# Optimization experiments

Measured on AMD Instinct MI355X. Metric: run time of the kernel, lower is better.

The kernel has to match this reference:

```python
import jax, jax.numpy as jnp
import numpy as np

IN_FEATURES = 4096
OUT_FEATURES = 11008
GROUP_SIZE = 128
NBITS = 4
ALPHA = 0.05  # relative noise scale: sigma = ALPHA * |w|


def setup_inputs() -> dict:
    key = jax.random.key(0)
    k_x, k_q, k_s, k_z, k_b, k_n = jax.random.split(key, 6)
    n_groups = IN_FEATURES // GROUP_SIZE  # 32
    x = jax.random.normal(k_x, (4096, IN_FEATURES), dtype=jnp.float32)
    qweight = jax.random.randint(k_q, (OUT_FEATURES, IN_FEATURES), 0, 2 ** NBITS, dtype=jnp.int32)
    scales = jax.random.uniform(k_s, (OUT_FEATURES, n_groups), dtype=jnp.float32) * 0.01 + 1e-4
    zeros = jax.random.uniform(k_z, (OUT_FEATURES, n_groups), dtype=jnp.float32) * (2 ** NBITS)
    bias = jax.random.normal(k_b, (OUT_FEATURES,), dtype=jnp.float32)
    noise = jax.random.normal(k_n, (OUT_FEATURES, IN_FEATURES), dtype=jnp.float32)
    return {"x": x, "qweight": qweight, "scales": scales, "zeros": zeros, "bias": bias, "noise": noise}


def _dequantize(qweight, scales, zeros):
    # grouped dequant: w[o, g*G + j] = (q - zero[o,g]) * scale[o,g]
    out_f, in_f = qweight.shape
    n_groups = scales.shape[1]
    qg = qweight.reshape(out_f, n_groups, GROUP_SIZE).astype(scales.dtype)
    w = (qg - zeros[:, :, None]) * scales[:, :, None]
    return w.reshape(out_f, in_f)


def reference(x, qweight, scales, zeros, bias, noise):
    w = _dequantize(qweight, scales, zeros)[:, :IN_FEATURES]
    sigma = ALPHA * jnp.abs(w)            # noise_fn(weight, alpha)
    w_noisy = (w + noise * sigma).astype(x.dtype)
    # F.linear: x @ w.T + bias
    return jnp.einsum('bi,oi->bo', x, w_noisy) + bias
```

## Files before the change

### kernel.cpp

```cpp
#include <hip/hip_runtime.h>
#include <hip/hip_bf16.h>
#include <stdint.h>

#define M_ROWS 4096
#define IN_F   4096
#define OUT_F  11008
#define N_GROUPS 32
#define ALPHA  0.05f

typedef __bf16 bf16;
typedef __bf16 bf16x8 __attribute__((ext_vector_type(8)));
typedef float  floatx4 __attribute__((ext_vector_type(4)));

__device__ __forceinline__ void async_copy16(const void* g, void* l) {
  __builtin_amdgcn_global_load_lds(
      (const __attribute__((address_space(1))) void*)g,
      (__attribute__((address_space(3))) void*)l, 16, 0, 0);
}

__global__ __launch_bounds__(256) void dequant_noise_kernel(
    const int* __restrict__ q, const float* __restrict__ scales,
    const float* __restrict__ zeros, const float* __restrict__ noise,
    bf16* __restrict__ wn) {
  int gid = blockIdx.x * 256 + threadIdx.x;
  int o = gid >> 9;
  int i = (gid & 511) << 3;
  int g = i >> 7;
  float s = scales[o * N_GROUPS + g];
  float z = zeros[o * N_GROUPS + g];
  size_t base = (size_t)o * IN_F + i;
  int4   q0 = *(const int4*)(q + base);
  int4   q1 = *(const int4*)(q + base + 4);
  float4 n0 = *(const float4*)(noise + base);
  float4 n1 = *(const float4*)(noise + base + 4);
  float qs[8] = {(float)q0.x, (float)q0.y, (float)q0.z, (float)q0.w,
                 (float)q1.x, (float)q1.y, (float)q1.z, (float)q1.w};
  float ns[8] = {n0.x, n0.y, n0.z, n0.w, n1.x, n1.y, n1.z, n1.w};
  bf16x8 out;
#pragma unroll
  for (int j = 0; j < 8; ++j) {
    float w = (qs[j] - z) * s;
    float v = fmaf(ALPHA * fabsf(w), ns[j], w);
    out[j] = (bf16)v;
  }
  *(bf16x8*)(wn + base) = out;
}

__global__ __launch_bounds__(256) void xcast_kernel(
    const float* __restrict__ x, bf16* __restrict__ xb) {
  size_t base = ((size_t)blockIdx.x * 256 + threadIdx.x) << 3;
  float4 a0 = *(const float4*)(x + base);
  float4 a1 = *(const float4*)(x + base + 4);
  float vs[8] = {a0.x, a0.y, a0.z, a0.w, a1.x, a1.y, a1.z, a1.w};
  bf16x8 out;
#pragma unroll
  for (int j = 0; j < 8; ++j) out[j] = (bf16)vs[j];
  *(bf16x8*)(xb + base) = out;
}

__global__ __launch_bounds__(256) void gemm_bt_kernel(
    const bf16* __restrict__ A,
    const bf16* __restrict__ W,
    const float* __restrict__ bias,
    float* __restrict__ C) {
  __shared__ bf16 ldsA[128 * 64];
  __shared__ bf16 ldsB[128 * 64];
  const int tid = threadIdx.x;
  const int wv = tid >> 6;
  const int ln = tid & 63;
  const int wr = wv >> 1;
  const int wc = wv & 1;
  const int mbase = blockIdx.y * 128;
  const int nbase = blockIdx.x * 128;

  const int srow = ln >> 3;
  const int scol = ((ln & 7) ^ srow) * 8;
  const int frow = ln & 15;
  const int g4   = ln >> 4;
  const int x7   = ln & 7;

  floatx4 acc[4][4] = {};

  for (int k0 = 0; k0 < IN_F; k0 += 64) {
#pragma unroll
    for (int t = 0; t < 4; ++t) {
      int rr = (wv * 4 + t) * 8 + srow;
      async_copy16(A + (size_t)(mbase + rr) * IN_F + k0 + scol,
                   &ldsA[(wv * 4 + t) * 512]);
      async_copy16(W + (size_t)(nbase + rr) * IN_F + k0 + scol,
                   &ldsB[(wv * 4 + t) * 512]);
    }
    __syncthreads();

#pragma unroll
    for (int kk = 0; kk < 64; kk += 32) {
      const int cb = kk >> 3;
      const int pc = (((cb + g4) ^ x7) << 3);
      bf16x8 af[4], bfr[4];
#pragma unroll
      for (int mi = 0; mi < 4; ++mi)
        af[mi] = *(const bf16x8*)&ldsA[(wr * 64 + mi * 16 + frow) * 64 + pc];
#pragma unroll
      for (int ni = 0; ni < 4; ++ni)
        bfr[ni] = *(const bf16x8*)&ldsB[(wc * 64 + ni * 16 + frow) * 64 + pc];
#pragma unroll
      for (int mi = 0; mi < 4; ++mi)
#pragma unroll
        for (int ni = 0; ni < 4; ++ni)
          acc[mi][ni] = __builtin_amdgcn_mfma_f32_16x16x32_bf16(
              af[mi], bfr[ni], acc[mi][ni], 0, 0, 0);
    }
    __syncthreads();
  }

#pragma unroll
  for (int ni = 0; ni < 4; ++ni) {
    int n = nbase + wc * 64 + ni * 16 + (ln & 15);
    float bv = bias[n];
#pragma unroll
    for (int mi = 0; mi < 4; ++mi) {
      int m0 = mbase + wr * 64 + mi * 16 + (ln >> 4) * 4;
#pragma unroll
      for (int r = 0; r < 4; ++r)
        C[(size_t)(m0 + r) * OUT_F + n] = acc[mi][ni][r] + bv;
    }
  }
}

extern "C" void kernel_launch(void* const* d_in, const int* in_sizes, int n_in,
                              void* d_out, int out_size, void* d_ws, size_t ws_size,
                              hipStream_t stream) {
  const float* x       = (const float*)d_in[0];
  const int*   qweight = (const int*)d_in[1];
  const float* scales  = (const float*)d_in[2];
  const float* zeros   = (const float*)d_in[3];
  const float* bias    = (const float*)d_in[4];
  const float* noise   = (const float*)d_in[5];
  float* out = (float*)d_out;

  bf16* wn = (bf16*)d_ws;
  bf16* xb = (bf16*)((char*)d_ws + (size_t)OUT_F * IN_F * sizeof(bf16));

  dequant_noise_kernel<<<(OUT_F * (IN_F / 8)) / 256, 256, 0, stream>>>(
      qweight, scales, zeros, noise, wn);
  xcast_kernel<<<(M_ROWS * (IN_F / 8)) / 256, 256, 0, stream>>>(x, xb);

  dim3 grid(OUT_F / 128, M_ROWS / 128);
  gemm_bt_kernel<<<grid, 256, 0, stream>>>(xb, wn, bias, out);
}
```

Measured before the change: 941.1 us.

## Replace GEMM with 256x256-tile, 4-stage async-LDS pipelined kernel

Replaces the 128x128 GEMM with a 512-thread kernel. Each block computes a 256x256 output tile using a 4-slot LDS ring filled by async global-to-LDS copies. Stages are issued three k-steps ahead, the A and B halves of each stage are interleaved with MFMA phases, and progress is coordinated with explicit vmcnt waits, barriers and setprio. A remapped 1D grid groups neighbouring M blocks for better L2 reuse. The aim is to hide global-load latency and cut LDS traffic per FLOP, at the cost of more registers, hand-tuned wait counts that must be exactly right, and a fragile custom swizzle layout.

New measurement: 774.7 us. -17.7%, faster.

```diff
diff --git a/kernel.cpp b/kernel.cpp
--- a/kernel.cpp
+++ b/kernel.cpp
@@ -58,68 +58,113 @@
   *(bf16x8*)(xb + base) = out;
 }
 
-__global__ __launch_bounds__(256) void gemm_bt_kernel(
+#define NH (IN_F / 32)
+
+__global__ __launch_bounds__(512, 2) void gemm_8ph_kernel(
     const bf16* __restrict__ A,
     const bf16* __restrict__ W,
     const float* __restrict__ bias,
     float* __restrict__ C) {
-  __shared__ bf16 ldsA[128 * 64];
-  __shared__ bf16 ldsB[128 * 64];
+  __shared__ bf16 lds[4 * 16384];
+
   const int tid = threadIdx.x;
   const int wv = tid >> 6;
   const int ln = tid & 63;
-  const int wr = wv >> 1;
-  const int wc = wv & 1;
-  const int mbase = blockIdx.y * 128;
-  const int nbase = blockIdx.x * 128;
+  const int wr = wv >> 2;
+  const int wc = wv & 3;
 
-  const int srow = ln >> 3;
-  const int scol = ((ln & 7) ^ srow) * 8;
+  const int orig = blockIdx.x;
+  const int idx  = orig >> 3;
+  const int bm   = ((orig & 7) << 1) | (idx & 1);
+  const int bn   = idx >> 1;
+  const int mbase = bm << 8;
+  const int nbase = bn << 8;
+
+  const int dec    = (ln & 7) ^ (ln >> 3);
+  const int rstage = wv * 32 + (ln >> 3) * 2 + (dec >> 2);
+  const int kcol   = (dec & 3) * 8;
+  const bf16* aS = A + (size_t)(mbase + rstage) * IN_F + kcol;
+  const bf16* bS = W + (size_t)(nbase + rstage) * IN_F + kcol;
+
   const int frow = ln & 15;
   const int g4   = ln >> 4;
-  const int x7   = ln & 7;
+  const int pc   = (((frow & 1) << 2) | g4) ^ (frow >> 1);
+  const int aoff = (wr * 64 + (frow >> 1)) * 64 + pc * 8;
+  const int boff = 8192 + (wc * 32 + (frow >> 1)) * 64 + pc * 8;
 
-  floatx4 acc[4][4] = {};
+  floatx4 acc[8][4] = {};
 
-  for (int k0 = 0; k0 < IN_F; k0 += 64) {
-#pragma unroll
-    for (int t = 0; t < 4; ++t) {
-      int rr = (wv * 4 + t) * 8 + srow;
-      async_copy16(A + (size_t)(mbase + rr) * IN_F + k0 + scol,
-                   &ldsA[(wv * 4 + t) * 512]);
-      async_copy16(W + (size_t)(nbase + rr) * IN_F + k0 + scol,
-                   &ldsB[(wv * 4 + t) * 512]);
-    }
-    __syncthreads();
+#define STAGE_A(DST, KH)                                                          \
+  do {                                                                            \
+    async_copy16(aS + (size_t)(KH) * 32,             &lds[(DST) * 16384 + wv * 1024]);        \
+    async_copy16(aS + (size_t)(KH) * 32 + 16 * IN_F, &lds[(DST) * 16384 + wv * 1024 + 512]);  \
+  } while (0)
+#define STAGE_B(DST, KH)                                                          \
+  do {                                                                            \
+    async_copy16(bS + (size_t)(KH) * 32,             &lds[(DST) * 16384 + 8192 + wv * 1024]);       \
+    async_copy16(bS + (size_t)(KH) * 32 + 16 * IN_F, &lds[(DST) * 16384 + 8192 + wv * 1024 + 512]); \
+  } while (0)
 
-#pragma unroll
-    for (int kk = 0; kk < 64; kk += 32) {
-      const int cb = kk >> 3;
-      const int pc = (((cb + g4) ^ x7) << 3);
-      bf16x8 af[4], bfr[4];
-#pragma unroll
-      for (int mi = 0; mi < 4; ++mi)
-        af[mi] = *(const bf16x8*)&ldsA[(wr * 64 + mi * 16 + frow) * 64 + pc];
-#pragma unroll
-      for (int ni = 0; ni < 4; ++ni)
-        bfr[ni] = *(const bf16x8*)&ldsB[(wc * 64 + ni * 16 + frow) * 64 + pc];
-#pragma unroll
-      for (int mi = 0; mi < 4; ++mi)
-#pragma unroll
-        for (int ni = 0; ni < 4; ++ni)
-          acc[mi][ni] = __builtin_amdgcn_mfma_f32_16x16x32_bf16(
-              af[mi], bfr[ni], acc[mi][ni], 0, 0, 0);
-    }
-    __syncthreads();
+  STAGE_A(0, 0); STAGE_B(0, 0);
+  STAGE_A(1, 1); STAGE_B(1, 1);
+  STAGE_A(2, 2); STAGE_B(2, 2);
+  asm volatile("s_waitcnt vmcnt(8)" ::: "memory");
+  __builtin_amdgcn_s_barrier();
+
+#define PAIR(SLOT, KH, DO_STAGE, TVM)                                             \
+  {                                                                               \
+    bf16x8 afr[4], bfr[4], afr2[4];                                               \
+    _Pragma("unroll") for (int mi = 0; mi < 4; ++mi)                              \
+      afr[mi] = *(const bf16x8*)&lds[(SLOT) * 16384 + aoff + mi * 512];           \
+    _Pragma("unroll") for (int ni = 0; ni < 4; ++ni)                              \
+      bfr[ni] = *(const bf16x8*)&lds[(SLOT) * 16384 + boff + ni * 512];           \
+    if (DO_STAGE) STAGE_A(((SLOT) + 3) & 3, (KH) + 3);                            \
+    __builtin_amdgcn_s_barrier();                                                 \
+    asm volatile("s_waitcnt lgkmcnt(0)" ::: "memory");                            \
+    __builtin_amdgcn_s_setprio(1);                                                \
+    _Pragma("unroll") for (int mi = 0; mi < 4; ++mi)                              \
+      _Pragma("unroll") for (int ni = 0; ni < 4; ++ni)                            \
+        acc[mi][ni] = __builtin_amdgcn_mfma_f32_16x16x32_bf16(                    \
+            afr[mi], bfr[ni], acc[mi][ni], 0, 0, 0);                              \
+    __builtin_amdgcn_s_setprio(0);                                                \
+    __builtin_amdgcn_s_barrier();                                                 \
+    _Pragma("unroll") for (int mi = 0; mi < 4; ++mi)                              \
+      afr2[mi] = *(const bf16x8*)&lds[(SLOT) * 16384 + aoff + (4 + mi) * 512];    \
+    if (DO_STAGE) STAGE_B(((SLOT) + 3) & 3, (KH) + 3);                            \
+    __builtin_amdgcn_s_barrier();                                                 \
+    asm volatile("s_waitcnt lgkmcnt(0)" ::: "memory");                            \
+    __builtin_amdgcn_s_setprio(1);                                                \
+    _Pragma("unroll") for (int mi = 0; mi < 4; ++mi)                              \
+      _Pragma("unroll") for (int ni = 0; ni < 4; ++ni)                            \
+        acc[4 + mi][ni] = __builtin_amdgcn_mfma_f32_16x16x32_bf16(                \
+            afr2[mi], bfr[ni], acc[4 + mi][ni], 0, 0, 0);                         \
+    __builtin_amdgcn_s_setprio(0);                                                \
+    asm volatile("s_waitcnt " TVM ::: "memory");                                  \
+    __builtin_amdgcn_s_barrier();                                                 \
   }
+
+  for (int kh = 0; kh < 124; kh += 4) {
+    PAIR(0, kh + 0, true, "vmcnt(8)");
+    PAIR(1, kh + 1, true, "vmcnt(8)");
+    PAIR(2, kh + 2, true, "vmcnt(8)");
+    PAIR(3, kh + 3, true, "vmcnt(8)");
+  }
+  PAIR(0, 124, true,  "vmcnt(8)");
+  PAIR(1, 125, false, "vmcnt(4)");
+  PAIR(2, 126, false, "vmcnt(0)");
+  PAIR(3, 127, false, "vmcnt(0)");
+
+#undef PAIR
+#undef STAGE_A
+#undef STAGE_B
 
 #pragma unroll
   for (int ni = 0; ni < 4; ++ni) {
     int n = nbase + wc * 64 + ni * 16 + (ln & 15);
     float bv = bias[n];
 #pragma unroll
-    for (int mi = 0; mi < 4; ++mi) {
-      int m0 = mbase + wr * 64 + mi * 16 + (ln >> 4) * 4;
+    for (int mi = 0; mi < 8; ++mi) {
+      int m0 = mbase + wr * 128 + mi * 16 + (ln >> 4) * 4;
 #pragma unroll
       for (int r = 0; r < 4; ++r)
         C[(size_t)(m0 + r) * OUT_F + n] = acc[mi][ni][r] + bv;
@@ -145,6 +190,5 @@
       qweight, scales, zeros, noise, wn);
   xcast_kernel<<<(M_ROWS * (IN_F / 8)) / 256, 256, 0, stream>>>(x, xb);
 
-  dim3 grid(OUT_F / 128, M_ROWS / 128);
-  gemm_bt_kernel<<<grid, 256, 0, stream>>>(xb, wn, bias, out);
+  gemm_8ph_kernel<<<dim3(688), 512, 0, stream>>>(xb, wn, bias, out);
 }
```
